# Kernel tuning notes

Measured on AMD Instinct MI355X. Metric: run time of the kernel, lower is better.

## Reference

```python
import jax, jax.numpy as jnp
import numpy as np

B, S, H = 2, 2048, 2048
N = 16               # num heads
NOPE, ROPE, V = 128, 64, 128
QHD = NOPE + ROPE    # 192 per-head q/k dim
QL, KVL = 1536, 512  # q_lora_rank, kv_lora_rank
THETA = 10000.0
SCALE = QHD ** -0.5
EPS = 1e-6


def rmsnorm(x, w):
    var = jnp.mean(x.astype(jnp.float32) ** 2, axis=-1, keepdims=True)
    return (x.astype(jnp.float32) * jax.lax.rsqrt(var + EPS)).astype(x.dtype) * w


def rotate_half(x):
    d = x.shape[-1] // 2
    return jnp.concatenate([-x[..., d:], x[..., :d]], axis=-1)


def setup_inputs() -> dict:
    key = jax.random.key(0)
    ks = jax.random.split(key, 8)
    w = lambda k, shape: jax.random.normal(k, shape, jnp.float32) * 0.02
    return {
        "hidden_states": jax.random.normal(ks[0], (B, S, H), jnp.float32),
        "position_ids": (jnp.arange(B * S, dtype=jnp.int64) % 4096).reshape(B, S),
        "q_a_w": w(ks[1], (QL, H)),
        "q_a_ln_w": jnp.ones((QL,), jnp.float32),
        "q_b_w": w(ks[2], (N * QHD, QL)),
        "kv_a_w": w(ks[3], (KVL + ROPE, H)),
        "kv_a_ln_w": jnp.ones((KVL,), jnp.float32),
        "kv_b_w": w(ks[4], (N * (NOPE + V), KVL)),
        "o_w": w(ks[5], (H, N * V)),
    }


def mla_forward(hidden_states, position_ids, q_a_w, q_a_ln_w, q_b_w,
                kv_a_w, kv_a_ln_w, kv_b_w, o_w):
    b, s, _ = hidden_states.shape
    # ---- Q low-rank path: q_b(rmsnorm(q_a(x))) ----
    q = rmsnorm(hidden_states @ q_a_w.T, q_a_ln_w) @ q_b_w.T
    q = q.reshape(b, s, N, QHD)
    q_nope, q_pe = q[..., :NOPE], q[..., NOPE:]
    # ---- compressed KV + shared rope key ----
    kv_a = hidden_states @ kv_a_w.T                       # [b,s,KVL+ROPE]
    compressed_kv = rmsnorm(kv_a[..., :KVL], kv_a_ln_w)   # [b,s,KVL]
    k_pe = kv_a[..., KVL:].reshape(b, s, 1, ROPE)         # MQA rope key
    # ---- RoPE (default, theta=1e4) from position_ids ----
    inv_freq = 1.0 / (THETA ** (jnp.arange(0, ROPE, 2, dtype=jnp.float32) / ROPE))
    freqs = position_ids.astype(jnp.float32)[..., None] * inv_freq  # [b,s,ROPE/2]
    emb = jnp.concatenate([freqs, freqs], axis=-1)                  # [b,s,ROPE]
    cos = jnp.cos(emb)[:, :, None, :].astype(hidden_states.dtype)   # [b,s,1,ROPE]
    sin = jnp.sin(emb)[:, :, None, :].astype(hidden_states.dtype)
    q_pe = q_pe * cos + rotate_half(q_pe) * sin
    k_pe = k_pe * cos + rotate_half(k_pe) * sin
    # ---- decompress latent KV via kv_b_proj ----
    kv = (compressed_kv @ kv_b_w.T).reshape(b, s, N, NOPE + V)
    k_nope, v = kv[..., :NOPE], kv[..., NOPE:]
    k = jnp.concatenate([k_nope, jnp.broadcast_to(k_pe, (b, s, N, ROPE))], axis=-1)
    qf = jnp.concatenate([q_nope, q_pe], axis=-1)          # [b,s,N,QHD]
    # ---- causal SDPA in bsnd layout ----
    scores = jnp.einsum('bqnd,bknd->bnqk', qf, k) * SCALE  # [b,N,s,s]
    causal = jnp.tril(jnp.ones((s, s), bool))
    scores = jnp.where(causal, scores, jnp.finfo(scores.dtype).min)
    probs = jax.nn.softmax(scores, axis=-1)
    attn = jnp.einsum('bnqk,bknd->bqnd', probs, v)         # [b,s,N,V]
    out = attn.reshape(b, s, N * V) @ o_w.T
    return out


def reference(hidden_states, position_ids, q_a_w, q_a_ln_w, q_b_w,
              kv_a_w, kv_a_ln_w, kv_b_w, o_w):
    return mla_forward(hidden_states, position_ids, q_a_w, q_a_ln_w, q_b_w,
                       kv_a_w, kv_a_ln_w, kv_b_w, o_w)
```

## Files before the change

### kernel.cpp

```cpp
#include <hip/hip_runtime.h>
#include <cstdio>

typedef unsigned short u16;
typedef u16 u16x8 __attribute__((ext_vector_type(8)));
typedef __bf16 bf16x8 __attribute__((ext_vector_type(8)));
typedef float f32x4 __attribute__((ext_vector_type(4)));

#define AS1 __attribute__((address_space(1)))
#define AS3 __attribute__((address_space(3)))

#define GLOAD16(gsrc, ldst) __builtin_amdgcn_global_load_lds( \
    (const AS1 void*)(gsrc), (AS3 void*)(ldst), 16, 0, 0)

__device__ __forceinline__ u16 f2bf(float f) {
  unsigned u = __builtin_bit_cast(unsigned, f);
  u += 0x7fffu + ((u >> 16) & 1u);
  return (u16)(u >> 16);
}
__device__ __forceinline__ float bf2f(u16 h) {
  return __builtin_bit_cast(float, (unsigned)h << 16);
}

__global__ __launch_bounds__(256) void cvt_pad_k(const float* __restrict__ src,
                                                 u16* __restrict__ dst,
                                                 long srcN, long dstN) {
  long i = ((long)blockIdx.x * 256 + threadIdx.x) * 8;
  const long stride = (long)gridDim.x * 256 * 8;
  for (; i < dstN; i += stride) {
    u16x8 o = {0,0,0,0,0,0,0,0};
    if (i < srcN) {
      const float4* p = (const float4*)(src + i);
      float4 a = p[0], b = p[1];
      o[0]=f2bf(a.x); o[1]=f2bf(a.y); o[2]=f2bf(a.z); o[3]=f2bf(a.w);
      o[4]=f2bf(b.x); o[5]=f2bf(b.y); o[6]=f2bf(b.z); o[7]=f2bf(b.w);
    }
    *(u16x8*)(dst + i) = o;
  }
}

__global__ __launch_bounds__(256) void rms_k(const u16* __restrict__ src, u16* __restrict__ dst,
                                             const float* __restrict__ w,
                                             int sstride, int dstride, int cols) {
  const int row = blockIdx.x;
  const int tid = threadIdx.x;
  const int nch = cols >> 3;
  float x[8];
  float ss = 0.f;
  if (tid < nch) {
    u16x8 v = *(const u16x8*)(src + (size_t)row * sstride + tid * 8);
#pragma unroll
    for (int j = 0; j < 8; ++j) { x[j] = bf2f(v[j]); ss += x[j] * x[j]; }
  } else {
#pragma unroll
    for (int j = 0; j < 8; ++j) x[j] = 0.f;
  }
#pragma unroll
  for (int off = 1; off < 64; off <<= 1) ss += __shfl_xor(ss, off);
  __shared__ float red[4];
  const int wv = tid >> 6, ln = tid & 63;
  if (ln == 0) red[wv] = ss;
  __syncthreads();
  const float tot = red[0] + red[1] + red[2] + red[3];
  const float rs = 1.0f / sqrtf(tot / (float)cols + 1e-6f);
  if (tid < nch) {
    u16x8 o;
#pragma unroll
    for (int j = 0; j < 8; ++j) o[j] = f2bf(x[j] * rs * w[tid * 8 + j]);
    *(u16x8*)(dst + (size_t)row * dstride + tid * 8) = o;
  }
}

__global__ __launch_bounds__(256) void rope_k(u16* __restrict__ q, const u16* __restrict__ kva,
                                              u16* __restrict__ kpe, const int* __restrict__ pos) {
  const int tok = blockIdx.x;
  const int j = threadIdx.x & 63;
  const int w = threadIdx.x >> 6;
  const float p = (float)pos[tok];
  const int jj = j & 31;
  const float inv = __powf(10000.0f, -(float)jj * (1.0f / 32.0f));
  float s, c;
  __sincosf(p * inv, &s, &c);
  const float sgn = (j < 32) ? -1.0f : 1.0f;
  const int partner = (j < 32) ? j + 32 : j - 32;
  if (w == 0) {
    const float x  = bf2f(kva[(size_t)tok * 640 + 512 + j]);
    const float xp = bf2f(kva[(size_t)tok * 640 + 512 + partner]);
    kpe[(size_t)tok * 64 + j] = f2bf(x * c + sgn * xp * s);
  }
#pragma unroll
  for (int hh = 0; hh < 4; ++hh) {
    const int h = w * 4 + hh;
    const size_t base = (size_t)tok * 3072 + h * 192 + 128;
    const float x  = bf2f(q[base + j]);
    const float xp = bf2f(q[base + partner]);
    q[base + j] = f2bf(x * c + sgn * xp * s);
  }
}

__global__ __launch_bounds__(256) void gemm_bt(const u16* __restrict__ A, const u16* __restrict__ B,
                                               u16* __restrict__ Cb, float* __restrict__ Cf,
                                               int M, int N, int K, float cs) {
  __shared__ __attribute__((aligned(16))) u16 As[128 * 64];
  __shared__ __attribute__((aligned(16))) u16 Bs[128 * 64];
  const int tid = threadIdx.x;
  const int m0 = blockIdx.y * 128, n0 = blockIdx.x * 128;
  const int w = tid >> 6, lane = tid & 63;
  const int wr = w >> 1, wc = w & 1;
  const int lr = lane & 15, g = lane >> 4;

  f32x4 acc[4][4] = {};

  for (int k0 = 0; k0 < K; k0 += 64) {
#pragma unroll
    for (int i = 0; i < 4; ++i) {
      const int c = i * 256 + tid;
      const int row = c >> 3, col = (c & 7) << 3;
      GLOAD16(A + (size_t)(m0 + row) * K + k0 + col, &As[c * 8]);
    }
#pragma unroll
    for (int i = 0; i < 4; ++i) {
      const int c = i * 256 + tid;
      const int row = c >> 3, col = (c & 7) << 3;
      GLOAD16(B + (size_t)(n0 + row) * K + k0 + col, &Bs[c * 8]);
    }
    __syncthreads();
    bf16x8 af[4][2], bfr[4][2];
#pragma unroll
    for (int x = 0; x < 4; ++x)
#pragma unroll
      for (int kk = 0; kk < 2; ++kk) {
        af[x][kk]  = *(const bf16x8*)(&As[(wr * 64 + x * 16 + lr) * 64 + kk * 32 + g * 8]);
        bfr[x][kk] = *(const bf16x8*)(&Bs[(wc * 64 + x * 16 + lr) * 64 + kk * 32 + g * 8]);
      }
#pragma unroll
    for (int mi = 0; mi < 4; ++mi)
#pragma unroll
      for (int ni = 0; ni < 4; ++ni)
#pragma unroll
        for (int kk = 0; kk < 2; ++kk)
          acc[mi][ni] = __builtin_amdgcn_mfma_f32_16x16x32_bf16(af[mi][kk], bfr[ni][kk],
                                                                acc[mi][ni], 0, 0, 0);
    __syncthreads();
  }

  const int rb = m0 + wr * 64, cb = n0 + wc * 64;
#pragma unroll
  for (int mi = 0; mi < 4; ++mi)
#pragma unroll
    for (int ni = 0; ni < 4; ++ni)
#pragma unroll
      for (int i = 0; i < 4; ++i) {
        const int r = rb + mi * 16 + g * 4 + i;
        const int cI = cb + ni * 16 + lr;
        if (Cf) Cf[(size_t)r * N + cI] = acc[mi][ni][i] * cs;
        else    Cb[(size_t)r * N + cI] = f2bf(acc[mi][ni][i] * cs);
      }
}

__global__ __launch_bounds__(512) void gemm256(const u16* __restrict__ A, const u16* __restrict__ B,
                                               u16* __restrict__ Cb, float* __restrict__ Cf,
                                               int M, int N, int K, float cs) {
  __shared__ __attribute__((aligned(16))) u16 As[2][256 * 64];
  __shared__ __attribute__((aligned(16))) u16 Bs[2][256 * 64];
  const int tid = threadIdx.x;
  const int m0 = blockIdx.y * 256, n0 = blockIdx.x * 256;
  const int wid = tid >> 6, lane = tid & 63;
  const int wr = wid >> 2, wc = wid & 3;
  const int lr = lane & 15, g = lane >> 4;

  const u16* pA[4];
  const u16* pB[4];
  int lOff[4];
#pragma unroll
  for (int i = 0; i < 4; ++i) {
    const int c = i * 512 + tid;
    const int row = c >> 3, cl = c & 7;
    const int cg = cl ^ (row & 7);
    lOff[i] = c * 8;
    pA[i] = A + (size_t)(m0 + row) * K + cg * 8;
    pB[i] = B + (size_t)(n0 + row) * K + cg * 8;
  }

  const int aBase = (wr * 128 + lr) * 64;
  const int bBase = (wc * 64 + lr) * 64;
  int kch[2];
#pragma unroll
  for (int kk = 0; kk < 2; ++kk) kch[kk] = ((kk * 4 + g) ^ (lr & 7)) * 8;

  f32x4 acc[8][4] = {};
  const int nkt = K >> 6;

#pragma unroll
  for (int i = 0; i < 4; ++i) GLOAD16(pA[i], &As[0][lOff[i]]);
#pragma unroll
  for (int i = 0; i < 4; ++i) GLOAD16(pB[i], &Bs[0][lOff[i]]);
#pragma unroll
  for (int i = 0; i < 4; ++i) { pA[i] += 64; pB[i] += 64; }
  asm volatile("s_waitcnt vmcnt(0)" ::: "memory");
  __builtin_amdgcn_s_barrier();
  __builtin_amdgcn_sched_barrier(0);

  for (int t = 0; t < nkt; ++t) {
    const int buf = t & 1;
    if (t + 1 < nkt) {
#pragma unroll
      for (int i = 0; i < 4; ++i) GLOAD16(pA[i], &As[buf ^ 1][lOff[i]]);
#pragma unroll
      for (int i = 0; i < 4; ++i) GLOAD16(pB[i], &Bs[buf ^ 1][lOff[i]]);
#pragma unroll
      for (int i = 0; i < 4; ++i) { pA[i] += 64; pB[i] += 64; }
    }
    bf16x8 bfr[4][2];
#pragma unroll
    for (int fn = 0; fn < 4; ++fn)
#pragma unroll
      for (int kk = 0; kk < 2; ++kk)
        bfr[fn][kk] = *(const bf16x8*)(&Bs[buf][bBase + fn * 1024 + kch[kk]]);
#pragma unroll
    for (int q = 0; q < 4; ++q) {
      bf16x8 afr[2][2];
#pragma unroll
      for (int fr = 0; fr < 2; ++fr)
#pragma unroll
        for (int kk = 0; kk < 2; ++kk)
          afr[fr][kk] = *(const bf16x8*)(&As[buf][aBase + (q * 2 + fr) * 1024 + kch[kk]]);
      asm volatile("s_waitcnt lgkmcnt(0)" ::: "memory");
      __builtin_amdgcn_sched_barrier(0);
      __builtin_amdgcn_s_setprio(1);
#pragma unroll
      for (int fr = 0; fr < 2; ++fr)
#pragma unroll
        for (int fn = 0; fn < 4; ++fn)
#pragma unroll
          for (int kk = 0; kk < 2; ++kk)
            acc[q * 2 + fr][fn] = __builtin_amdgcn_mfma_f32_16x16x32_bf16(
                afr[fr][kk], bfr[fn][kk], acc[q * 2 + fr][fn], 0, 0, 0);
      __builtin_amdgcn_s_setprio(0);
      if (q == 3) asm volatile("s_waitcnt vmcnt(0)" ::: "memory");
      __builtin_amdgcn_s_barrier();
    }
    __builtin_amdgcn_sched_barrier(0);
  }

  const int rb = m0 + wr * 128, cb = n0 + wc * 64;
#pragma unroll
  for (int fm = 0; fm < 8; ++fm)
#pragma unroll
    for (int fn = 0; fn < 4; ++fn)
#pragma unroll
      for (int i = 0; i < 4; ++i) {
        const int r = rb + fm * 16 + g * 4 + i;
        const int cI = cb + fn * 16 + lr;
        if (Cf) Cf[(size_t)r * N + cI] = acc[fm][fn][i] * cs;
        else    Cb[(size_t)r * N + cI] = f2bf(acc[fm][fn][i] * cs);
      }
}

__global__ __launch_bounds__(256) void vtr_k(const u16* __restrict__ kvb, u16* __restrict__ vT) {
  __shared__ u16 tile[128 * 72];
  const int bh = blockIdx.x, b = bh >> 4, h = bh & 15;
  const int s0 = blockIdx.y * 64;
  const int t = threadIdx.x;
  {
    const int s = t >> 2;
    const int vc = (t & 3) * 32;
    const u16* src = kvb + (size_t)(b * 2048 + s0 + s) * 4096 + h * 256 + 128 + vc;
#pragma unroll
    for (int c = 0; c < 4; ++c) {
      u16x8 v = *(const u16x8*)(src + c * 8);
#pragma unroll
      for (int e = 0; e < 8; ++e) tile[(vc + c * 8 + e) * 72 + s] = v[e];
    }
  }
  __syncthreads();
  {
    const int v = t >> 1;
    const int sh = (t & 1) * 32;
    u16* dst = vT + (size_t)(bh * 128 + v) * 2048 + s0 + sh;
    const u16* srow = &tile[v * 72 + sh];
#pragma unroll
    for (int c = 0; c < 4; ++c)
      *(u16x8*)(dst + c * 8) = *(const u16x8*)(srow + c * 8);
  }
}

__global__ __launch_bounds__(256) void attn_k(const u16* __restrict__ q, const u16* __restrict__ kvb,
                                              const u16* __restrict__ kpe, const u16* __restrict__ vT,
                                              u16* __restrict__ ao) {
  __shared__ __attribute__((aligned(16))) u16 Ks[64 * 192];
  __shared__ __attribute__((aligned(16))) u16 Vt[128 * 64];

  const int bh = blockIdx.x;
  const int b = bh >> 4, h = bh & 15;
  const int j = 15 - blockIdx.y;
  const int tid = threadIdx.x, w = tid >> 6, lane = tid & 63;
  const int lr = lane & 15, g = lane >> 4;

  const int q0 = j * 128;
  const int qrb = q0 + w * 32;
  u16* Psw = &Ks[w * 2304];

  bf16x8 qf[2][6];
#pragma unroll
  for (int m = 0; m < 2; ++m)
#pragma unroll
    for (int kd = 0; kd < 6; ++kd)
      qf[m][kd] = *(const bf16x8*)(q + (size_t)(b * 2048 + qrb + m * 16 + lr) * 3072 +
                                   h * 192 + kd * 32 + g * 8);

  float mrow[2][4], lrow[2][4];
  f32x4 o[2][8] = {};
#pragma unroll
  for (int m = 0; m < 2; ++m)
#pragma unroll
    for (int i = 0; i < 4; ++i) { mrow[m][i] = -1e30f; lrow[m][i] = 0.f; }

  const int nt = (q0 >> 6) + 2;
  for (int t = 0; t < nt; ++t) {
    const int k0 = t * 64;
#pragma unroll
    for (int i = 0; i < 6; ++i) {
      const int c = i * 256 + tid;
      const int row = c / 24, cl = c - row * 24;
      const int cg = cl ^ (row & 7);
      const u16* src = (cg < 16)
        ? (kvb + (size_t)(b * 2048 + k0 + row) * 4096 + h * 256 + cg * 8)
        : (kpe + (size_t)(b * 2048 + k0 + row) * 64 + (cg - 16) * 8);
      GLOAD16(src, &Ks[c * 8]);
    }
#pragma unroll
    for (int i = 0; i < 4; ++i) {
      const int c = i * 256 + tid;
      const int v = c >> 3, cl = c & 7;
      const int cg = cl ^ (v & 7);
      GLOAD16(vT + (size_t)(bh * 128 + v) * 2048 + k0 + cg * 8, &Vt[c * 8]);
    }
    __syncthreads();

    const bool active = (k0 <= qrb + 31);
    f32x4 sAcc[2][4] = {};
    if (active) {
      __builtin_amdgcn_s_setprio(1);
#pragma unroll
      for (int nf = 0; nf < 4; ++nf) {
        const int rr = nf * 16 + lr;
#pragma unroll
        for (int kd = 0; kd < 6; ++kd) {
          const int ch = (kd * 4 + g) ^ (rr & 7);
          const bf16x8 kf = *(const bf16x8*)(&Ks[rr * 192 + ch * 8]);
#pragma unroll
          for (int m = 0; m < 2; ++m)
            sAcc[m][nf] = __builtin_amdgcn_mfma_f32_16x16x32_bf16(qf[m][kd], kf, sAcc[m][nf], 0, 0, 0);
        }
      }
      __builtin_amdgcn_s_setprio(0);
    }
    __syncthreads();

    if (active) {
      const bool needMask = (k0 + 63 > qrb);
#pragma unroll
      for (int m = 0; m < 2; ++m) {
        float sv[4][4];
        if (needMask) {
#pragma unroll
          for (int nf = 0; nf < 4; ++nf)
#pragma unroll
            for (int i = 0; i < 4; ++i) {
              const int qrow = qrb + m * 16 + g * 4 + i;
              const int kcol = k0 + nf * 16 + lr;
              sv[nf][i] = (kcol > qrow) ? -1e30f : sAcc[m][nf][i];
            }
        } else {
#pragma unroll
          for (int nf = 0; nf < 4; ++nf)
#pragma unroll
            for (int i = 0; i < 4; ++i) sv[nf][i] = sAcc[m][nf][i];
        }
        float rm4[4];
        bool exceed = false;
#pragma unroll
        for (int i = 0; i < 4; ++i) {
          float rm = fmaxf(fmaxf(sv[0][i], sv[1][i]), fmaxf(sv[2][i], sv[3][i]));
          rm = fmaxf(rm, __shfl_xor(rm, 1));
          rm = fmaxf(rm, __shfl_xor(rm, 2));
          rm = fmaxf(rm, __shfl_xor(rm, 4));
          rm = fmaxf(rm, __shfl_xor(rm, 8));
          rm4[i] = rm;
          exceed = exceed || (rm > mrow[m][i] + 8.0f);
        }
        if (__any(exceed)) {
#pragma unroll
          for (int i = 0; i < 4; ++i) {
            const float mn = fmaxf(mrow[m][i], rm4[i]);
            const float fac = __expf(mrow[m][i] - mn);
            mrow[m][i] = mn;
            lrow[m][i] *= fac;
#pragma unroll
            for (int nv = 0; nv < 8; ++nv) o[m][nv][i] *= fac;
          }
        }
#pragma unroll
        for (int i = 0; i < 4; ++i) {
          float rsum = 0.f;
#pragma unroll
          for (int nf = 0; nf < 4; ++nf) { sv[nf][i] = __expf(sv[nf][i] - mrow[m][i]); rsum += sv[nf][i]; }
          rsum += __shfl_xor(rsum, 1);
          rsum += __shfl_xor(rsum, 2);
          rsum += __shfl_xor(rsum, 4);
          rsum += __shfl_xor(rsum, 8);
          lrow[m][i] += rsum;
        }
#pragma unroll
        for (int nf = 0; nf < 4; ++nf)
#pragma unroll
          for (int i = 0; i < 4; ++i)
            Psw[(m * 16 + g * 4 + i) * 72 + nf * 16 + lr] = f2bf(sv[nf][i]);
      }
      asm volatile("s_waitcnt lgkmcnt(0)" ::: "memory");

      __builtin_amdgcn_s_setprio(1);
#pragma unroll
      for (int kc = 0; kc < 2; ++kc) {
        bf16x8 vfr[8];
#pragma unroll
        for (int nv = 0; nv < 8; ++nv) {
          const int v = nv * 16 + lr;
          const int cx = (kc * 4 + g) ^ (v & 7);
          vfr[nv] = *(const bf16x8*)(&Vt[v * 64 + cx * 8]);
        }
#pragma unroll
        for (int m = 0; m < 2; ++m) {
          const bf16x8 pf = *(const bf16x8*)(&Psw[(m * 16 + lr) * 72 + kc * 32 + g * 8]);
#pragma unroll
          for (int nv = 0; nv < 8; ++nv)
            o[m][nv] = __builtin_amdgcn_mfma_f32_16x16x32_bf16(pf, vfr[nv], o[m][nv], 0, 0, 0);
        }
      }
      __builtin_amdgcn_s_setprio(0);
    }
    __syncthreads();
  }

#pragma unroll
  for (int m = 0; m < 2; ++m)
#pragma unroll
    for (int i = 0; i < 4; ++i) {
      const float inv = 1.0f / lrow[m][i];
      const size_t tokOff = (size_t)(b * 2048 + qrb + m * 16 + g * 4 + i) * 2048 + h * 128;
#pragma unroll
      for (int nv = 0; nv < 8; ++nv)
        ao[tokOff + nv * 16 + lr] = f2bf(o[m][nv][i] * inv);
    }
}

extern "C" void kernel_launch(void* const* d_in, const int* in_sizes, int n_in,
                              void* d_out, int out_size, void* d_ws, size_t ws_size,
                              hipStream_t stream) {
  const float* hidden  = (const float*)d_in[0];
  const int*   pos     = (const int*)d_in[1];
  const float* q_a_w   = (const float*)d_in[2];
  const float* q_a_ln  = (const float*)d_in[3];
  const float* q_b_w   = (const float*)d_in[4];
  const float* kv_a_w  = (const float*)d_in[5];
  const float* kv_a_ln = (const float*)d_in[6];
  const float* kv_b_w  = (const float*)d_in[7];
  const float* o_w     = (const float*)d_in[8];
  float* out = (float*)d_out;

  char* ws = (char*)d_ws;
  u16* hb  = (u16*)(ws + 0L);
  u16* w1  = (u16*)(ws + 16777216L);
  u16* w2  = (u16*)(ws + 23068672L);
  u16* w3  = (u16*)(ws + 32505856L);
  u16* w4  = (u16*)(ws + 35127296L);
  u16* w5  = (u16*)(ws + 39321600L);
  u16* qa  = (u16*)(ws + 47710208L);
  u16* qb  = (u16*)(ws + 60293120L);
  u16* kva = (u16*)(ws + 85458944L);
  u16* ckv = (u16*)(ws + 90701824L);
  u16* kpe = (u16*)(ws + 94896128L);
  u16* kvb = (u16*)(ws + 95420416L);
  u16* ao  = (u16*)(ws + 128974848L);
  u16* vT  = hb;
  if (ws_size < 145752064UL) { fprintf(stderr, "ws too small: %zu\n", ws_size); return; }

  const float SCALE = 0.07216878364870323f;

  auto cvt = [&](const float* s, u16* d, long sn, long dn) {
    long blocks = (dn / 8 + 255) / 256; if (blocks > 2048) blocks = 2048;
    cvt_pad_k<<<dim3((unsigned)blocks), dim3(256), 0, stream>>>(s, d, sn, dn);
  };
  cvt(hidden, hb, 4096L * 2048, 4096L * 2048);
  cvt(q_a_w,  w1, 1536L * 2048, 1536L * 2048);
  cvt(q_b_w,  w2, 3072L * 1536, 3072L * 1536);
  cvt(kv_a_w, w3, 576L * 2048,  640L * 2048);
  cvt(kv_b_w, w4, 4096L * 512,  4096L * 512);
  cvt(o_w,    w5, 2048L * 2048, 2048L * 2048);

  gemm_bt<<<dim3(12, 32), 256, 0, stream>>>(hb, w1, qa, nullptr, 4096, 1536, 2048, 1.0f);
  rms_k<<<4096, 256, 0, stream>>>(qa, qa, q_a_ln, 1536, 1536, 1536);
  gemm256<<<dim3(12, 16), 512, 0, stream>>>(qa, w2, qb, nullptr, 4096, 3072, 1536, SCALE);
  gemm_bt<<<dim3(5, 32), 256, 0, stream>>>(hb, w3, kva, nullptr, 4096, 640, 2048, 1.0f);
  rms_k<<<4096, 256, 0, stream>>>(kva, ckv, kv_a_ln, 640, 512, 512);
  rope_k<<<4096, 256, 0, stream>>>(qb, kva, kpe, pos);
  gemm256<<<dim3(16, 16), 512, 0, stream>>>(ckv, w4, kvb, nullptr, 4096, 4096, 512, 1.0f);
  vtr_k<<<dim3(32, 32), 256, 0, stream>>>(kvb, vT);
  attn_k<<<dim3(32, 16), 256, 0, stream>>>(qb, kvb, kpe, vT, ao);
  gemm256<<<dim3(8, 16), 512, 0, stream>>>(ao, w5, nullptr, out, 4096, 2048, 2048, 1.0f);
}
```

Baseline: 456.9 us.

## Fuse q_a and kv_a projections into one GEMM; give attention a separate P buffer

Concatenates the q_a and kv_a weights so one GEMM of width 2176 computes both low-rank projections from the hidden states, and the two RMSNorms read from that shared output. In the attention kernel the P tile gets its own shared buffer instead of aliasing the K tile. This removes the barrier between QK and softmax, and the per-tile load addresses are precomputed and advanced incrementally. The kvb data is addressed as a fixed offset from kpe based on the workspace layout. This is fragile and raises shared-memory use, which may lower occupancy.

Result: faster. 432.9 us (-5.3%).

```diff
diff --git a/kernel.cpp b/kernel.cpp
--- a/kernel.cpp
+++ b/kernel.cpp
@@ -70,7 +70,7 @@
   }
 }
 
-__global__ __launch_bounds__(256) void rope_k(u16* __restrict__ q, const u16* __restrict__ kva,
+__global__ __launch_bounds__(256) void rope_k(u16* __restrict__ q, const u16* __restrict__ qk_a,
                                               u16* __restrict__ kpe, const int* __restrict__ pos) {
   const int tok = blockIdx.x;
   const int j = threadIdx.x & 63;
@@ -83,8 +83,8 @@
   const float sgn = (j < 32) ? -1.0f : 1.0f;
   const int partner = (j < 32) ? j + 32 : j - 32;
   if (w == 0) {
-    const float x  = bf2f(kva[(size_t)tok * 640 + 512 + j]);
-    const float xp = bf2f(kva[(size_t)tok * 640 + 512 + partner]);
+    const float x  = bf2f(qk_a[(size_t)tok * 2176 + 2048 + j]);
+    const float xp = bf2f(qk_a[(size_t)tok * 2176 + 2048 + partner]);
     kpe[(size_t)tok * 64 + j] = f2bf(x * c + sgn * xp * s);
   }
 #pragma unroll
@@ -284,11 +284,11 @@
   }
 }
 
-__global__ __launch_bounds__(256) void attn_k(const u16* __restrict__ q, const u16* __restrict__ kvb,
-                                              const u16* __restrict__ kpe, const u16* __restrict__ vT,
-                                              u16* __restrict__ ao) {
+__global__ __launch_bounds__(256) void attn_k(const u16* __restrict__ q, const u16* __restrict__ kpe,
+                                              const u16* __restrict__ vT, u16* __restrict__ ao) {
   __shared__ __attribute__((aligned(16))) u16 Ks[64 * 192];
   __shared__ __attribute__((aligned(16))) u16 Vt[128 * 64];
+  __shared__ __attribute__((aligned(16))) u16 Ps[4][32 * 72];
 
   const int bh = blockIdx.x;
   const int b = bh >> 4, h = bh & 15;
@@ -298,7 +298,29 @@
 
   const int q0 = j * 128;
   const int qrb = q0 + w * 32;
-  u16* Psw = &Ks[w * 2304];
+  u16* Psw = &Ps[w][0];
+
+  int koff[6], kstep[6], kld[6];
+#pragma unroll
+  for (int i = 0; i < 6; ++i) {
+    const int c = i * 256 + tid;
+    const int row = c / 24, cl = c - row * 24;
+    const int cg = cl ^ (row & 7);
+    kld[i] = c * 8;
+    if (cg < 16) { koff[i] = 262144 + (b * 2048 + row) * 4096 + h * 256 + cg * 8;
+                   kstep[i] = 64 * 4096; }
+    else         { koff[i] = (b * 2048 + row) * 64 + (cg - 16) * 8;
+                   kstep[i] = 64 * 64; }
+  }
+  int voff[4], vld[4];
+#pragma unroll
+  for (int i = 0; i < 4; ++i) {
+    const int c = i * 256 + tid;
+    const int v = c >> 3, cl = c & 7;
+    const int cg = cl ^ (v & 7);
+    vld[i] = c * 8;
+    voff[i] = (bh * 128 + v) * 2048 + cg * 8;
+  }
 
   bf16x8 qf[2][6];
 #pragma unroll
@@ -320,26 +342,19 @@
     const int k0 = t * 64;
 #pragma unroll
     for (int i = 0; i < 6; ++i) {
-      const int c = i * 256 + tid;
-      const int row = c / 24, cl = c - row * 24;
-      const int cg = cl ^ (row & 7);
-      const u16* src = (cg < 16)
-        ? (kvb + (size_t)(b * 2048 + k0 + row) * 4096 + h * 256 + cg * 8)
-        : (kpe + (size_t)(b * 2048 + k0 + row) * 64 + (cg - 16) * 8);
-      GLOAD16(src, &Ks[c * 8]);
+      GLOAD16(kpe + koff[i], &Ks[kld[i]]);
+      koff[i] += kstep[i];
     }
 #pragma unroll
     for (int i = 0; i < 4; ++i) {
-      const int c = i * 256 + tid;
-      const int v = c >> 3, cl = c & 7;
-      const int cg = cl ^ (v & 7);
-      GLOAD16(vT + (size_t)(bh * 128 + v) * 2048 + k0 + cg * 8, &Vt[c * 8]);
+      GLOAD16(vT + voff[i], &Vt[vld[i]]);
+      voff[i] += 64;
     }
     __syncthreads();
 
     const bool active = (k0 <= qrb + 31);
-    f32x4 sAcc[2][4] = {};
     if (active) {
+      f32x4 sAcc[2][4] = {};
       __builtin_amdgcn_s_setprio(1);
 #pragma unroll
       for (int nf = 0; nf < 4; ++nf) {
@@ -354,10 +369,7 @@
         }
       }
       __builtin_amdgcn_s_setprio(0);
-    }
-    __syncthreads();
-
-    if (active) {
+
       const bool needMask = (k0 + 63 > qrb);
 #pragma unroll
       for (int m = 0; m < 2; ++m) {
@@ -470,18 +482,17 @@
 
   char* ws = (char*)d_ws;
   u16* hb  = (u16*)(ws + 0L);
-  u16* w1  = (u16*)(ws + 16777216L);
-  u16* w2  = (u16*)(ws + 23068672L);
-  u16* w3  = (u16*)(ws + 32505856L);
+  u16* wA  = (u16*)(ws + 16777216L);
+  u16* w2  = (u16*)(ws + 25690112L);
   u16* w4  = (u16*)(ws + 35127296L);
   u16* w5  = (u16*)(ws + 39321600L);
   u16* qa  = (u16*)(ws + 47710208L);
   u16* qb  = (u16*)(ws + 60293120L);
-  u16* kva = (u16*)(ws + 85458944L);
-  u16* ckv = (u16*)(ws + 90701824L);
-  u16* kpe = (u16*)(ws + 94896128L);
-  u16* kvb = (u16*)(ws + 95420416L);
-  u16* ao  = (u16*)(ws + 128974848L);
+  u16* ckv = (u16*)(ws + 85458944L);
+  u16* kpe = (u16*)(ws + 89653248L);
+  u16* kvb = (u16*)(ws + 90177536L);
+  u16* ao  = (u16*)(ws + 123731968L);
+  u16* qk_a = kvb;
   u16* vT  = hb;
   if (ws_size < 145752064UL) { fprintf(stderr, "ws too small: %zu\n", ws_size); return; }
 
@@ -492,20 +503,19 @@
     cvt_pad_k<<<dim3((unsigned)blocks), dim3(256), 0, stream>>>(s, d, sn, dn);
   };
   cvt(hidden, hb, 4096L * 2048, 4096L * 2048);
-  cvt(q_a_w,  w1, 1536L * 2048, 1536L * 2048);
+  cvt(q_a_w,  wA, 1536L * 2048, 1536L * 2048);
+  cvt(kv_a_w, wA + 1536L * 2048, 576L * 2048, 640L * 2048);
   cvt(q_b_w,  w2, 3072L * 1536, 3072L * 1536);
-  cvt(kv_a_w, w3, 576L * 2048,  640L * 2048);
   cvt(kv_b_w, w4, 4096L * 512,  4096L * 512);
   cvt(o_w,    w5, 2048L * 2048, 2048L * 2048);
 
-  gemm_bt<<<dim3(12, 32), 256, 0, stream>>>(hb, w1, qa, nullptr, 4096, 1536, 2048, 1.0f);
-  rms_k<<<4096, 256, 0, stream>>>(qa, qa, q_a_ln, 1536, 1536, 1536);
+  gemm_bt<<<dim3(17, 32), 256, 0, stream>>>(hb, wA, qk_a, nullptr, 4096, 2176, 2048, 1.0f);
+  rms_k<<<4096, 256, 0, stream>>>(qk_a, qa, q_a_ln, 2176, 1536, 1536);
+  rms_k<<<4096, 256, 0, stream>>>(qk_a + 1536, ckv, kv_a_ln, 2176, 512, 512);
   gemm256<<<dim3(12, 16), 512, 0, stream>>>(qa, w2, qb, nullptr, 4096, 3072, 1536, SCALE);
-  gemm_bt<<<dim3(5, 32), 256, 0, stream>>>(hb, w3, kva, nullptr, 4096, 640, 2048, 1.0f);
-  rms_k<<<4096, 256, 0, stream>>>(kva, ckv, kv_a_ln, 640, 512, 512);
-  rope_k<<<4096, 256, 0, stream>>>(qb, kva, kpe, pos);
+  rope_k<<<4096, 256, 0, stream>>>(qb, qk_a, kpe, pos);
   gemm256<<<dim3(16, 16), 512, 0, stream>>>(ckv, w4, kvb, nullptr, 4096, 4096, 512, 1.0f);
   vtr_k<<<dim3(32, 32), 256, 0, stream>>>(kvb, vT);
-  attn_k<<<dim3(32, 16), 256, 0, stream>>>(qb, kvb, kpe, vT, ao);
+  attn_k<<<dim3(32, 16), 256, 0, stream>>>(qb, kpe, vT, ao);
   gemm256<<<dim3(8, 16), 512, 0, stream>>>(ao, w5, nullptr, out, 4096, 2048, 2048, 1.0f);
 }
```
